# Kernel tuning notes

Measured on AMD Instinct MI355X. Metric: run time of the kernel, lower is better.

The kernel has to match this reference:

```python
import jax, jax.numpy as jnp
import numpy as np

C, DI, N, K, R = 64, 128, 16, 4, 4   # d_model, d_inner, d_state, d_conv, dt_rank
B, H, W = 4, 96, 96


def _layer_params(key):
    ks = jax.random.split(key, 6)
    p = {}
    p['ln_g'] = jnp.ones((C,), jnp.float32)
    p['ln_b'] = jnp.zeros((C,), jnp.float32)
    p['in_w'] = jax.random.normal(ks[0], (2 * DI, C), jnp.float32) / np.sqrt(C)
    p['conv_w'] = jax.random.normal(ks[1], (DI, K), jnp.float32) / np.sqrt(K)
    p['conv_b'] = jnp.zeros((DI,), jnp.float32)
    p['xp_w'] = jax.random.normal(ks[2], (R + 2 * N, DI), jnp.float32) / np.sqrt(DI)
    p['dt_w'] = jax.random.normal(ks[3], (DI, R), jnp.float32) / np.sqrt(R)
    p['dt_b'] = jnp.full((DI,), -4.0, jnp.float32)  # softplus(-4) ~ 0.018, sane dt
    p['A_log'] = jnp.broadcast_to(jnp.log(jnp.arange(1, N + 1, dtype=jnp.float32)), (DI, N)) + jnp.zeros((DI, N), jnp.float32)
    p['D'] = jnp.ones((DI,), jnp.float32)
    p['out_w'] = jax.random.normal(ks[4], (C, DI), jnp.float32) / np.sqrt(DI)
    p['skip'] = jnp.ones((1,), jnp.float32)
    p['pr_w'] = jax.random.normal(ks[5], (C, C), jnp.float32) / np.sqrt(C)
    p['pr_b'] = jnp.zeros((C,), jnp.float32)
    return p


def setup_inputs() -> dict:
    key = jax.random.key(0)
    k0, k1, k2 = jax.random.split(key, 3)
    inp = {'x': jax.random.normal(k0, (B, C, H, W), jnp.float32)}
    for i, k in ((1, k1), (2, k2)):
        for n, v in _layer_params(k).items():
            inp[f'{n}{i}'] = v
    return inp


def _silu(x):
    return x * jax.nn.sigmoid(x)


def _layer_norm(x, g, b, eps=1e-5):
    m = x.mean(-1, keepdims=True)
    v = x.var(-1, keepdims=True)
    return (x - m) * jax.lax.rsqrt(v + eps) * g + b


def _instance_norm(x, eps=1e-5):  # x: [B, C, H, W], no affine
    m = x.mean((2, 3), keepdims=True)
    v = x.var((2, 3), keepdims=True)
    return (x - m) * jax.lax.rsqrt(v + eps)


def _causal_conv(x, w, b):  # x: [B, L, D]; w: [D, K] depthwise; causal pad left
    L = x.shape[1]
    xp = jnp.pad(x, ((0, 0), (K - 1, 0), (0, 0)))
    y = b
    for k in range(K):
        y = y + xp[:, k:k + L, :] * w[:, k]
    return y


def _mamba(x, in_w, conv_w, conv_b, xp_w, dt_w, dt_b, A_log, Dp, out_w):
    # x: [B, L, C]
    xz = x @ in_w.T                       # [B, L, 2*DI]
    xin, z = jnp.split(xz, 2, axis=-1)
    xc = _silu(_causal_conv(xin, conv_w, conv_b))   # [B, L, DI]
    dbl = xc @ xp_w.T                     # [B, L, R + 2N]
    dt, Bm, Cm = jnp.split(dbl, [R, R + N], axis=-1)
    dt = jax.nn.softplus(dt @ dt_w.T + dt_b)        # [B, L, DI]
    A = -jnp.exp(A_log)                   # [DI, N]
    a = jnp.exp(dt[..., None] * A)                        # [B, L, DI, N]
    bb = dt[..., None] * Bm[:, :, None, :] * xc[..., None]  # [B, L, DI, N]

    def comb(l, r):
        a1, b1 = l
        a2, b2 = r
        return (a1 * a2, a2 * b1 + b2)

    _, h = jax.lax.associative_scan(comb, (a, bb), axis=1)  # h: [B, L, DI, N]
    y = jnp.einsum('bldn,bln->bld', h, Cm) + Dp * xc
    y = y * _silu(z)
    return y @ out_w.T                    # [B, L, C]


def _mamba_layer(x4, p):
    # x4: [B, C, H, W]
    b, c, h, w = x4.shape
    xf = x4.reshape(b, c, h * w).transpose(0, 2, 1)   # [B, L, C]
    xn = _layer_norm(xf, p['ln_g'], p['ln_b'])
    xm = _mamba(xn, p['in_w'], p['conv_w'], p['conv_b'], p['xp_w'], p['dt_w'],
                p['dt_b'], p['A_log'], p['D'], p['out_w']) + p['skip'] * xf
    xm = xm @ p['pr_w'].T + p['pr_b']
    return xm.transpose(0, 2, 1).reshape(b, c, h, w)


_PNAMES = ['ln_g', 'ln_b', 'in_w', 'conv_w', 'conv_b', 'xp_w', 'dt_w', 'dt_b',
           'A_log', 'D', 'out_w', 'skip', 'pr_w', 'pr_b']


def _forward(x, *ps):
    p1 = dict(zip(_PNAMES, ps[:14]))
    p2 = dict(zip(_PNAMES, ps[14:]))
    identity = x
    h = jax.nn.relu(_instance_norm(x))
    h = _mamba_layer(h, p1)
    h = jax.nn.relu(_instance_norm(h))
    h = _mamba_layer(h, p2)
    return h + identity


def reference(x, ln_g1, ln_b1, in_w1, conv_w1, conv_b1, xp_w1, dt_w1, dt_b1,
              A_log1, D1, out_w1, skip1, pr_w1, pr_b1,
              ln_g2, ln_b2, in_w2, conv_w2, conv_b2, xp_w2, dt_w2, dt_b2,
              A_log2, D2, out_w2, skip2, pr_w2, pr_b2):
    return _forward(x, ln_g1, ln_b1, in_w1, conv_w1, conv_b1, xp_w1, dt_w1, dt_b1,
                    A_log1, D1, out_w1, skip1, pr_w1, pr_b1,
                    ln_g2, ln_b2, in_w2, conv_w2, conv_b2, xp_w2, dt_w2, dt_b2,
                    A_log2, D2, out_w2, skip2, pr_w2, pr_b2)
```

## Files before the change

kernel.cpp:

```cpp
#include <hip/hip_runtime.h>
#include <math.h>

#define BB 4
#define CC 64
#define DI 128
#define NS 16
#define LL 9216
#define NT (LL / 64)

#define GCH 576
#define LCH 16
#define NSEQ 8192
#define SD  512
#define NG 24
#define GS 24

typedef __attribute__((ext_vector_type(8))) short bf16x8;
typedef __attribute__((ext_vector_type(4))) float fx4;
#define MFMA16 __builtin_amdgcn_mfma_f32_16x16x32_bf16

static __device__ __forceinline__ unsigned short f2b(float f) {
  unsigned u = __float_as_uint(f);
  u += 0x7fffu + ((u >> 16) & 1u);
  return (unsigned short)(u >> 16);
}
static __device__ __forceinline__ float b2f(unsigned short s) {
  return __uint_as_float(((unsigned)s) << 16);
}
static __device__ __forceinline__ float silu_f(float x) {
  return x / (1.f + __expf(-x));
}

static __device__ __forceinline__ void powers16(float e1, float* a) {
  float p2 = e1 * e1, p4 = p2 * p2, p8 = p4 * p4;
  a[0] = e1;      a[1] = p2;      a[2] = p2 * e1;      a[3] = p4;
  a[4] = p4 * e1; a[5] = p4 * p2; a[6] = p4 * p2 * e1; a[7] = p8;
  a[8] = p8 * e1; a[9] = p8 * p2; a[10] = p8 * p2 * e1; a[11] = p8 * p4;
  a[12] = p8 * p4 * e1; a[13] = p8 * p4 * p2; a[14] = p8 * p4 * p2 * e1; a[15] = p8 * p8;
}

static __device__ __forceinline__ float dt_and_a(float v, float A0, bool aone, bool afast,
                                                 const float* __restrict__ Alog, int d,
                                                 float* a) {
  float em = __expf(-fabsf(v));
  float t = 1.f + em;
  float dtv = fmaxf(v, 0.f) + __logf(t);
  if (aone) {
    float e1 = ((v >= 0.f) ? em : 1.f) / t;
    powers16(e1, a);
  } else if (afast) {
    powers16(__expf(dtv * A0), a);
  } else {
    #pragma unroll
    for (int n = 0; n < 16; ++n) a[n] = __expf(dtv * -__expf(Alog[d * NS + n]));
  }
  return dtv;
}

__global__ __launch_bounds__(256) void k_cvt(const float* __restrict__ inw1, const float* __restrict__ xpw1,
                                             const float* __restrict__ ow1, const float* __restrict__ pw1,
                                             const float* __restrict__ inw2, const float* __restrict__ xpw2,
                                             const float* __restrict__ ow2, const float* __restrict__ pw2,
                                             const float* __restrict__ alog1, const float* __restrict__ alog2,
                                             unsigned short* __restrict__ wb,
                                             float* __restrict__ prep) {
  int blk = blockIdx.x;
  int tid = threadIdx.x;
  if (blk >= 272) {
    int layer = blk - 272;
    const float* alog = layer ? alog2 : alog1;
    float* pr = prep + layer * 2304;
    #pragma unroll
    for (int j = 0; j < 8; ++j) {
      int e = tid + 256 * j;
      pr[e] = -__expf(alog[e]);
    }
    if (tid < 128) {
      int d = tid;
      float A0 = -__expf(alog[d * NS]);
      bool afast = true;
      #pragma unroll
      for (int n = 1; n < 16; ++n) {
        float An = -__expf(alog[d * NS + n]);
        afast = afast && (fabsf(An - A0 * (float)(n + 1)) <= 1e-3f * (float)(n + 1) * fabsf(A0));
      }
      bool aone = afast && (A0 == -1.0f);
      pr[2048 + d] = A0;
      pr[2176 + d] = aone ? 2.f : (afast ? 1.f : 0.f);
    }
    return;
  }
  int idx = blk * 256 + tid;
  int layer = idx >= 34816;
  int e = idx - layer * 34816;
  const float* inw = layer ? inw2 : inw1;
  const float* xpw = layer ? xpw2 : xpw1;
  const float* ow = layer ? ow2 : ow1;
  const float* pw = layer ? pw2 : pw1;
  float v;
  if (e < 16384) v = inw[e];
  else if (e < 22528) { int t = e - 16384; int r = t >> 7, c = t & 127; v = (r < 36) ? xpw[r * 128 + c] : 0.f; }
  else if (e < 30720) v = ow[e - 22528];
  else v = pw[e - 30720];
  wb[idx] = f2b(v);
}

__global__ __launch_bounds__(256) void k_stats(const float* __restrict__ p,
                                               float* __restrict__ stats) {
  int bc = blockIdx.x;
  const float* row = p + (size_t)bc * LL;
  float s = 0.f, s2 = 0.f;
  for (int i = threadIdx.x; i < LL; i += 256) {
    float v = row[i];
    s += v; s2 += v * v;
  }
  #pragma unroll
  for (int o = 32; o > 0; o >>= 1) {
    s += __shfl_down(s, o);
    s2 += __shfl_down(s2, o);
  }
  __shared__ float red[8];
  int w = threadIdx.x >> 6;
  if ((threadIdx.x & 63) == 0) { red[w] = s; red[4 + w] = s2; }
  __syncthreads();
  if (threadIdx.x == 0) {
    float S = red[0] + red[1] + red[2] + red[3];
    float S2 = red[4] + red[5] + red[6] + red[7];
    float m = S * (1.f / LL);
    float var = S2 * (1.f / LL) - m * m;
    stats[bc * 2] = m;
    stats[bc * 2 + 1] = rsqrtf(var + 1e-5f);
  }
}

__global__ __launch_bounds__(256) void k_fusein(const float* __restrict__ p,
                                                const float* __restrict__ stats,
                                                const float* __restrict__ g,
                                                const float* __restrict__ be,
                                                const unsigned short* __restrict__ w_b,
                                                unsigned short* __restrict__ xf_b,
                                                unsigned short* __restrict__ xin_b,
                                                unsigned short* __restrict__ sz_b) {
  int b = blockIdx.x / NT;
  int l0 = (blockIdx.x % NT) * 64;
  __shared__ float T[64][65];
  __shared__ unsigned short Tb[64][72];
  int li = threadIdx.x & 63;
  int c0 = threadIdx.x >> 6;
  #pragma unroll
  for (int j = 0; j < 16; ++j) {
    int c = c0 * 16 + j;
    float m = stats[(b * CC + c) * 2];
    float rs = stats[(b * CC + c) * 2 + 1];
    float v = p[((size_t)(b * CC + c)) * LL + l0 + li];
    T[li][c] = fmaxf((v - m) * rs, 0.f);
  }
  __syncthreads();
  {
    int row = threadIdx.x >> 2, part = threadIdx.x & 3;
    int ch0 = part * 16;
    float s = 0.f, s2 = 0.f;
    #pragma unroll
    for (int j = 0; j < 16; ++j) {
      float v = T[row][ch0 + j];
      s += v; s2 += v * v;
    }
    s += __shfl_xor(s, 1); s2 += __shfl_xor(s2, 1);
    s += __shfl_xor(s, 2); s2 += __shfl_xor(s2, 2);
    float m = s * (1.f / 64.f);
    float var = s2 * (1.f / 64.f) - m * m;
    float rs = rsqrtf(var + 1e-5f);
    size_t off0 = ((size_t)b * LL + l0 + row) * CC + ch0;
    #pragma unroll
    for (int j4 = 0; j4 < 4; ++j4) {
      float4 v4 = *(float4*)&T[row][ch0 + j4 * 4];
      xf_b[off0 + j4 * 4 + 0] = f2b(v4.x);
      xf_b[off0 + j4 * 4 + 1] = f2b(v4.y);
      xf_b[off0 + j4 * 4 + 2] = f2b(v4.z);
      xf_b[off0 + j4 * 4 + 3] = f2b(v4.w);
      float4 g4 = *(const float4*)&g[ch0 + j4 * 4];
      float4 b4 = *(const float4*)&be[ch0 + j4 * 4];
      Tb[row][ch0 + j4 * 4 + 0] = f2b((v4.x - m) * rs * g4.x + b4.x);
      Tb[row][ch0 + j4 * 4 + 1] = f2b((v4.y - m) * rs * g4.y + b4.y);
      Tb[row][ch0 + j4 * 4 + 2] = f2b((v4.z - m) * rs * g4.z + b4.z);
      Tb[row][ch0 + j4 * 4 + 3] = f2b((v4.w - m) * rs * g4.w + b4.w);
    }
  }
  __syncthreads();
  int lane = threadIdx.x & 63;
  int wv = threadIdx.x >> 6;
  int lr = lane & 15, kg = lane >> 4;
  int m0 = wv * 16;
  int rowg0 = blockIdx.x * 64 + m0;
  bf16x8 a0 = *(const bf16x8*)&Tb[m0 + lr][kg * 8];
  bf16x8 a1 = *(const bf16x8*)&Tb[m0 + lr][32 + kg * 8];
  #pragma unroll
  for (int nt = 0; nt < 16; ++nt) {
    bf16x8 b0 = *(const bf16x8*)&w_b[(size_t)(nt * 16 + lr) * CC + kg * 8];
    bf16x8 b1 = *(const bf16x8*)&w_b[(size_t)(nt * 16 + lr) * CC + 32 + kg * 8];
    fx4 c = {0.f, 0.f, 0.f, 0.f};
    c = MFMA16(a0, b0, c, 0, 0, 0);
    c = MFMA16(a1, b1, c, 0, 0, 0);
    #pragma unroll
    for (int r = 0; r < 4; ++r) {
      int row = rowg0 + kg * 4 + r, col = nt * 16 + lr;
      if (col < 128) xin_b[(size_t)row * DI + col] = f2b(c[r]);
      else           sz_b[(size_t)row * DI + col - 128] = f2b(silu_f(c[r]));
    }
  }
}

__global__ __launch_bounds__(128) void k_scanAX(const unsigned short* __restrict__ xin_b,
                                                const float* __restrict__ cw,
                                                const float* __restrict__ cb,
                                                const unsigned short* __restrict__ xpw_b,
                                                const float* __restrict__ Alog,
                                                const float* __restrict__ prep,
                                                const float* __restrict__ dtw,
                                                const float* __restrict__ dtbp,
                                                const float* __restrict__ Dp,
                                                float* __restrict__ dblC,
                                                float* __restrict__ dts,
                                                unsigned short* __restrict__ hlb,
                                                unsigned short* __restrict__ y1b,
                                                unsigned short* __restrict__ dtpreb) {
  int g = blockIdx.x % GCH;
  int b = blockIdx.x / GCH;
  __shared__ float dblP[2][16][40];
  __shared__ unsigned short xcS[16][136];
  int wv = threadIdx.x >> 6, lane = threadIdx.x & 63;
  int lr = lane & 15, kg = lane >> 4;
  {
    int lloc = g * LCH + lr;
    size_t row = (size_t)b * LL + lloc;
    const bf16x8 zv8 = {0, 0, 0, 0, 0, 0, 0, 0};
    fx4 acc[3];
    #pragma unroll
    for (int nt = 0; nt < 3; ++nt) acc[nt] = (fx4){0.f, 0.f, 0.f, 0.f};
    #pragma unroll
    for (int kk = 0; kk < 2; ++kk) {
      int cbase = (wv * 2 + kk) * 32 + kg * 8;
      bf16x8 x3 = *(const bf16x8*)&xin_b[row * DI + cbase];
      bf16x8 x2 = (lloc >= 1) ? *(const bf16x8*)&xin_b[(row - 1) * DI + cbase] : zv8;
      bf16x8 x1 = (lloc >= 2) ? *(const bf16x8*)&xin_b[(row - 2) * DI + cbase] : zv8;
      bf16x8 x0 = (lloc >= 3) ? *(const bf16x8*)&xin_b[(row - 3) * DI + cbase] : zv8;
      bf16x8 a;
      #pragma unroll
      for (int e = 0; e < 8; ++e) {
        int dd = cbase + e;
        float4 w4 = *(const float4*)&cw[dd * 4];
        float v = cb[dd] + b2f((unsigned short)x0[e]) * w4.x + b2f((unsigned short)x1[e]) * w4.y
                + b2f((unsigned short)x2[e]) * w4.z + b2f((unsigned short)x3[e]) * w4.w;
        a[e] = (short)f2b(silu_f(v));
      }
      *(bf16x8*)&xcS[lr][cbase] = a;
      #pragma unroll
      for (int nt = 0; nt < 3; ++nt) {
        bf16x8 bfr = *(const bf16x8*)&xpw_b[(size_t)(nt * 16 + lr) * DI + cbase];
        acc[nt] = MFMA16(a, bfr, acc[nt], 0, 0, 0);
      }
    }
    #pragma unroll
    for (int nt = 0; nt < 3; ++nt)
      #pragma unroll
      for (int r = 0; r < 4; ++r) {
        int col = nt * 16 + lr;
        if (col < 36) dblP[wv][kg * 4 + r][col] = acc[nt][r];
      }
  }
  __syncthreads();
  for (int e = threadIdx.x; e < 576; e += 128) {
    int r = e / 36, c = e - r * 36;
    dblP[0][r][c] += dblP[1][r][c];
  }
  __syncthreads();
  {
    size_t cbase16 = ((size_t)b * LL + g * LCH) * 16;
    #pragma unroll
    for (int j = 0; j < 2; ++j) {
      int e = threadIdx.x + 128 * j;
      dblC[cbase16 + e] = dblP[0][e >> 4][20 + (e & 15)];
    }
  }
  int d = threadIdx.x;
  float A0 = prep[2048 + d];
  int fl = (int)prep[2176 + d];
  bool afast = fl >= 1;
  bool aone = fl == 2;
  float4 w4 = *(const float4*)&dtw[d * 4];
  float dtbv = dtbp[d];
  float Dv = Dp[d];
  float h[16];
  #pragma unroll
  for (int n = 0; n < 16; ++n) h[n] = 0.f;
  float dtsum = 0.f;
  size_t sbase = ((size_t)b * LL + g * LCH) * DI + d;
  #pragma unroll 4
  for (int l = 0; l < LCH; ++l) {
    float xcv = b2f(xcS[l][d]);
    float4 qv = *(float4*)&dblP[0][l][0];
    float v = dtbv + qv.x * w4.x + qv.y * w4.y + qv.z * w4.z + qv.w * w4.w;
    float a[16];
    float dtv = dt_and_a(v, A0, aone, afast, Alog, d, a);
    float dx = dtv * xcv;
    dtsum += dtv;
    float4 b0 = *(float4*)&dblP[0][l][4];
    float4 b1 = *(float4*)&dblP[0][l][8];
    float4 b2 = *(float4*)&dblP[0][l][12];
    float4 b3 = *(float4*)&dblP[0][l][16];
    h[0]  = a[0]  * h[0]  + dx * b0.x;  h[1]  = a[1]  * h[1]  + dx * b0.y;
    h[2]  = a[2]  * h[2]  + dx * b0.z;  h[3]  = a[3]  * h[3]  + dx * b0.w;
    h[4]  = a[4]  * h[4]  + dx * b1.x;  h[5]  = a[5]  * h[5]  + dx * b1.y;
    h[6]  = a[6]  * h[6]  + dx * b1.z;  h[7]  = a[7]  * h[7]  + dx * b1.w;
    h[8]  = a[8]  * h[8]  + dx * b2.x;  h[9]  = a[9]  * h[9]  + dx * b2.y;
    h[10] = a[10] * h[10] + dx * b2.z;  h[11] = a[11] * h[11] + dx * b2.w;
    h[12] = a[12] * h[12] + dx * b3.x;  h[13] = a[13] * h[13] + dx * b3.y;
    h[14] = a[14] * h[14] + dx * b3.z;  h[15] = a[15] * h[15] + dx * b3.w;
    float4 cc0 = *(float4*)&dblP[0][l][20];
    float4 cc1 = *(float4*)&dblP[0][l][24];
    float4 cc2 = *(float4*)&dblP[0][l][28];
    float4 cc3 = *(float4*)&dblP[0][l][32];
    float y0 = h[0] * cc0.x + h[1] * cc0.y + h[2] * cc0.z + h[3] * cc0.w;
    float y1 = h[4] * cc1.x + h[5] * cc1.y + h[6] * cc1.z + h[7] * cc1.w;
    float y2 = h[8] * cc2.x + h[9] * cc2.y + h[10] * cc2.z + h[11] * cc2.w;
    float y3 = h[12] * cc3.x + h[13] * cc3.y + h[14] * cc3.z + h[15] * cc3.w;
    y1b[sbase + (size_t)l * DI] = f2b((y0 + y1) + (y2 + y3) + Dv * xcv);
    dtpreb[sbase + (size_t)l * DI] = f2b(dtsum);
  }
  dts[(size_t)g * SD + b * DI + d] = dtsum;
  size_t o = (size_t)g * NSEQ + ((size_t)b * DI + d) * NS;
  bf16x8 hv0, hv1;
  #pragma unroll
  for (int n = 0; n < 8; ++n) { hv0[n] = (short)f2b(h[n]); hv1[n] = (short)f2b(h[8 + n]); }
  *(bf16x8*)&hlb[o] = hv0;
  *(bf16x8*)&hlb[o + 8] = hv1;
}

__global__ __launch_bounds__(256) void k_scan2a(const float* __restrict__ dts,
                                                const unsigned short* __restrict__ hlb,
                                                const float* __restrict__ prep,
                                                float* __restrict__ gap,
                                                float* __restrict__ ghl) {
  int t = blockIdx.x * 256 + threadIdx.x;
  int grp = t >> 13, seq = t & (NSEQ - 1);
  int sd = seq >> 4;
  float An = prep[seq & (DI * NS - 1)];
  float A = 1.f, H = 0.f;
  int c0 = grp * GS;
  #pragma unroll 4
  for (int c = 0; c < GS; ++c) {
    float a = __expf(An * dts[(size_t)(c0 + c) * SD + sd]);
    H = a * H + b2f(hlb[(size_t)(c0 + c) * NSEQ + seq]);
    A *= a;
  }
  gap[t] = A;
  ghl[t] = H;
}

__global__ __launch_bounds__(256) void k_scan2bc(const float* __restrict__ dts,
                                                 const unsigned short* __restrict__ hlb,
                                                 const float* __restrict__ gap,
                                                 const float* __restrict__ ghl,
                                                 const float* __restrict__ prep,
                                                 unsigned short* __restrict__ hib) {
  int t = blockIdx.x * 256 + threadIdx.x;
  int grp = t >> 13, seq = t & (NSEQ - 1);
  int sd = seq >> 4;
  float An = prep[seq & (DI * NS - 1)];
  float h = 0.f;
  for (int gg = 0; gg < grp; ++gg)
    h = gap[gg * NSEQ + seq] * h + ghl[gg * NSEQ + seq];
  int c0 = grp * GS;
  #pragma unroll 4
  for (int c = 0; c < GS; ++c) {
    float a = __expf(An * dts[(size_t)(c0 + c) * SD + sd]);
    hib[(size_t)(c0 + c) * NSEQ + seq] = f2b(h);
    h = a * h + b2f(hlb[(size_t)(c0 + c) * NSEQ + seq]);
  }
}

__global__ __launch_bounds__(128) void k_scanCO(const float* __restrict__ dblC,
                                                const unsigned short* __restrict__ sz_b,
                                                const unsigned short* __restrict__ y1b,
                                                const unsigned short* __restrict__ dtpreb,
                                                const float* __restrict__ Alog,
                                                const float* __restrict__ prep,
                                                const unsigned short* __restrict__ hib,
                                                const unsigned short* __restrict__ ow_b,
                                                const unsigned short* __restrict__ xf_b,
                                                const float* __restrict__ skipv,
                                                const unsigned short* __restrict__ pw_b,
                                                const float* __restrict__ pb,
                                                const float* __restrict__ ident,
                                                float* __restrict__ dst, int addid) {
  int g = blockIdx.x % GCH;
  int b = blockIdx.x / GCH;
  int d = threadIdx.x;
  __shared__ float Cms[LCH * NS];
  __shared__ unsigned short yS[16][136];
  __shared__ unsigned short tmpS[16][72];
  {
    int tid = threadIdx.x;
    size_t cb16 = ((size_t)b * LL + g * LCH) * 16;
    if (tid < 64) *(float4*)&Cms[tid * 4] = *(const float4*)&dblC[cb16 + tid * 4];
  }
  float A0 = prep[2048 + d];
  bool afast = ((int)prep[2176 + d]) >= 1;
  __syncthreads();
  size_t o = (size_t)g * NSEQ + ((size_t)b * DI + d) * NS;
  float hiR[16];
  {
    bf16x8 h0 = *(const bf16x8*)&hib[o];
    bf16x8 h1 = *(const bf16x8*)&hib[o + 8];
    #pragma unroll
    for (int n = 0; n < 8; ++n) {
      hiR[n] = b2f((unsigned short)h0[n]);
      hiR[8 + n] = b2f((unsigned short)h1[n]);
    }
  }
  size_t base = ((size_t)b * LL + g * LCH) * DI + d;
  #pragma unroll 4
  for (int l = 0; l < LCH; ++l) {
    float dtpre = b2f(dtpreb[base + (size_t)l * DI]);
    float y1v = b2f(y1b[base + (size_t)l * DI]);
    float sg = b2f(sz_b[base + (size_t)l * DI]);
    float pw[16];
    if (afast) {
      powers16(__expf(A0 * dtpre), pw);
    } else {
      #pragma unroll
      for (int n = 0; n < 16; ++n) pw[n] = __expf(-__expf(Alog[d * NS + n]) * dtpre);
    }
    float4 c0 = *(float4*)&Cms[l * 16];
    float4 c1 = *(float4*)&Cms[l * 16 + 4];
    float4 c2 = *(float4*)&Cms[l * 16 + 8];
    float4 c3 = *(float4*)&Cms[l * 16 + 12];
    float s0 = c0.x * pw[0] * hiR[0] + c0.y * pw[1] * hiR[1] + c0.z * pw[2] * hiR[2] + c0.w * pw[3] * hiR[3];
    float s1 = c1.x * pw[4] * hiR[4] + c1.y * pw[5] * hiR[5] + c1.z * pw[6] * hiR[6] + c1.w * pw[7] * hiR[7];
    float s2 = c2.x * pw[8] * hiR[8] + c2.y * pw[9] * hiR[9] + c2.z * pw[10] * hiR[10] + c2.w * pw[11] * hiR[11];
    float s3 = c3.x * pw[12] * hiR[12] + c3.y * pw[13] * hiR[13] + c3.z * pw[14] * hiR[14] + c3.w * pw[15] * hiR[15];
    float yv = y1v + ((s0 + s1) + (s2 + s3));
    yS[l][d] = f2b(yv * sg);
  }
  __syncthreads();
  int lane = threadIdx.x & 63;
  int lr = lane & 15, kg = lane >> 4;
  int lw = threadIdx.x >> 6;
  {
    fx4 oacc[2];
    oacc[0] = (fx4){0.f, 0.f, 0.f, 0.f};
    oacc[1] = (fx4){0.f, 0.f, 0.f, 0.f};
    #pragma unroll
    for (int ks = 0; ks < 4; ++ks) {
      int cbase = ks * 32 + kg * 8;
      bf16x8 a = *(const bf16x8*)&yS[lr][cbase];
      #pragma unroll
      for (int j = 0; j < 2; ++j) {
        int nt = lw * 2 + j;
        bf16x8 bfr = *(const bf16x8*)&ow_b[(size_t)(nt * 16 + lr) * DI + cbase];
        oacc[j] = MFMA16(a, bfr, oacc[j], 0, 0, 0);
      }
    }
    float sk = skipv[0];
    #pragma unroll
    for (int j = 0; j < 2; ++j) {
      int nt = lw * 2 + j;
      #pragma unroll
      for (int r = 0; r < 4; ++r) {
        int rowl = kg * 4 + r, col = nt * 16 + lr;
        size_t grow = (size_t)b * LL + g * LCH + rowl;
        tmpS[rowl][col] = f2b(oacc[j][r] + sk * b2f(xf_b[grow * CC + col]));
      }
    }
  }
  __syncthreads();
  {
    fx4 pacc[2];
    pacc[0] = (fx4){0.f, 0.f, 0.f, 0.f};
    pacc[1] = (fx4){0.f, 0.f, 0.f, 0.f};
    #pragma unroll
    for (int ks = 0; ks < 2; ++ks) {
      int cbase = ks * 32 + kg * 8;
      bf16x8 bfrag = *(const bf16x8*)&tmpS[lr][cbase];
      #pragma unroll
      for (int j = 0; j < 2; ++j) {
        int ct = lw * 2 + j;
        bf16x8 a = *(const bf16x8*)&pw_b[(size_t)(ct * 16 + lr) * CC + cbase];
        pacc[j] = MFMA16(a, bfrag, pacc[j], 0, 0, 0);
      }
    }
    #pragma unroll
    for (int j = 0; j < 2; ++j) {
      int ct = lw * 2 + j;
      #pragma unroll
      for (int r = 0; r < 4; ++r) {
        int c = ct * 16 + kg * 4 + r;
        int lpos = g * LCH + lr;
        size_t off = ((size_t)(b * CC + c)) * LL + lpos;
        float val = pacc[j][r] + pb[c];
        if (addid) val += ident[off];
        dst[off] = val;
      }
    }
  }
}

extern "C" void kernel_launch(void* const* d_in, const int* in_sizes, int n_in,
                              void* d_out, int out_size, void* d_ws, size_t ws_size,
                              hipStream_t stream) {
  const float* x = (const float*)d_in[0];
  float* ws = (float*)d_ws;
  float* stats = ws;
  unsigned short* xf_b   = (unsigned short*)(ws + 1024);
  unsigned short* xin_b  = (unsigned short*)(ws + 1180672);
  unsigned short* sz_b   = (unsigned short*)(ws + 3539968);
  float* dblC  = ws + 5899264;
  float* dts   = ws + 6489088;
  unsigned short* hlb    = (unsigned short*)(ws + 6784000);
  unsigned short* hib    = (unsigned short*)(ws + 9143296);
  float* gap   = ws + 11502592;
  float* ghl   = ws + 11699200;
  unsigned short* wb     = (unsigned short*)(ws + 11895808);
  unsigned short* y1b    = (unsigned short*)(ws + 11930624);
  unsigned short* dtpreb = (unsigned short*)(ws + 14289920);
  float* prep  = ws + 16649216;
  float* inter = (float*)hlb;
  float* outp  = (float*)d_out;

  k_cvt<<<274, 256, 0, stream>>>((const float*)d_in[3], (const float*)d_in[6],
                                 (const float*)d_in[11], (const float*)d_in[13],
                                 (const float*)d_in[17], (const float*)d_in[20],
                                 (const float*)d_in[25], (const float*)d_in[27],
                                 (const float*)d_in[9], (const float*)d_in[23],
                                 wb, prep);

  const float* cur = x;
  for (int layer = 0; layer < 2; ++layer) {
    const int p0 = 1 + 14 * layer;
    const float* ln_g   = (const float*)d_in[p0 + 0];
    const float* ln_b   = (const float*)d_in[p0 + 1];
    const float* conv_w = (const float*)d_in[p0 + 3];
    const float* conv_b = (const float*)d_in[p0 + 4];
    const float* dt_w   = (const float*)d_in[p0 + 6];
    const float* dt_b   = (const float*)d_in[p0 + 7];
    const float* A_log  = (const float*)d_in[p0 + 8];
    const float* Dp     = (const float*)d_in[p0 + 9];
    const float* skip   = (const float*)d_in[p0 + 11];
    const float* pr_b   = (const float*)d_in[p0 + 13];
    const unsigned short* inw_b = wb + (size_t)layer * 34816;
    const unsigned short* xpw_b = inw_b + 16384;
    const unsigned short* ow_b  = inw_b + 22528;
    const unsigned short* pw_b  = inw_b + 30720;
    const float* prepL = prep + (size_t)layer * 2304;
    float* dst = (layer == 0) ? inter : outp;

    k_stats  <<<BB * CC, 256, 0, stream>>>(cur, stats);
    k_fusein <<<BB * NT, 256, 0, stream>>>(cur, stats, ln_g, ln_b, inw_b, xf_b, xin_b, sz_b);
    k_scanAX <<<BB * GCH, 128, 0, stream>>>(xin_b, conv_w, conv_b, xpw_b, A_log, prepL,
                                            dt_w, dt_b, Dp, dblC, dts, hlb, y1b, dtpreb);
    k_scan2a <<<(NG * NSEQ) / 256, 256, 0, stream>>>(dts, hlb, prepL, gap, ghl);
    k_scan2bc<<<(NG * NSEQ) / 256, 256, 0, stream>>>(dts, hlb, gap, ghl, prepL, hib);
    k_scanCO <<<BB * GCH, 128, 0, stream>>>(dblC, sz_b, y1b, dtpreb, A_log, prepL, hib,
                                            ow_b, xf_b, skip, pw_b, pr_b, x, dst, layer);
    cur = inter;
  }
}
```

Measured before the change: 208.2 us.

## Fuse instance-norm statistics into weight-convert and scan output kernels

The first layer's per-channel mean and rstd are now computed by extra blocks in the weight-conversion kernel, so the separate stats pass over the input runs alongside it. For the second layer, the output kernel of layer one writes per-chunk partial sums and sums of squares, and a small finalize kernel reduces them. This removes a full re-read of the intermediate activation and one launch per layer. The cost is extra shuffles and partial-sum writes in the scan output epilogue, a new workspace buffer, and a different summation order in the statistics.

```diff
diff --git a/kernel.cpp b/kernel.cpp
--- a/kernel.cpp
+++ b/kernel.cpp
@@ -62,10 +62,39 @@
                                              const float* __restrict__ inw2, const float* __restrict__ xpw2,
                                              const float* __restrict__ ow2, const float* __restrict__ pw2,
                                              const float* __restrict__ alog1, const float* __restrict__ alog2,
+                                             const float* __restrict__ x,
                                              unsigned short* __restrict__ wb,
-                                             float* __restrict__ prep) {
+                                             float* __restrict__ prep,
+                                             float* __restrict__ stats) {
   int blk = blockIdx.x;
   int tid = threadIdx.x;
+  if (blk >= 274) {
+    int bc = blk - 274;
+    const float* row = x + (size_t)bc * LL;
+    float s = 0.f, s2 = 0.f;
+    for (int i = tid; i < LL; i += 256) {
+      float v = row[i];
+      s += v; s2 += v * v;
+    }
+    #pragma unroll
+    for (int o = 32; o > 0; o >>= 1) {
+      s += __shfl_down(s, o);
+      s2 += __shfl_down(s2, o);
+    }
+    __shared__ float red[8];
+    int w = tid >> 6;
+    if ((tid & 63) == 0) { red[w] = s; red[4 + w] = s2; }
+    __syncthreads();
+    if (tid == 0) {
+      float S = red[0] + red[1] + red[2] + red[3];
+      float S2 = red[4] + red[5] + red[6] + red[7];
+      float m = S * (1.f / LL);
+      float var = S2 * (1.f / LL) - m * m;
+      stats[bc * 2] = m;
+      stats[bc * 2 + 1] = rsqrtf(var + 1e-5f);
+    }
+    return;
+  }
   if (blk >= 272) {
     int layer = blk - 272;
     const float* alog = layer ? alog2 : alog1;
@@ -105,27 +134,23 @@
   wb[idx] = f2b(v);
 }
 
-__global__ __launch_bounds__(256) void k_stats(const float* __restrict__ p,
-                                               float* __restrict__ stats) {
+__global__ __launch_bounds__(64) void k_statfin(const float* __restrict__ partials,
+                                                float* __restrict__ stats) {
   int bc = blockIdx.x;
-  const float* row = p + (size_t)bc * LL;
-  float s = 0.f, s2 = 0.f;
-  for (int i = threadIdx.x; i < LL; i += 256) {
-    float v = row[i];
-    s += v; s2 += v * v;
+  int b = bc >> 6, c = bc & 63;
+  int t = threadIdx.x;
+  float S = 0.f, S2 = 0.f;
+  for (int g = t; g < GCH; g += 64) {
+    size_t pbase = ((size_t)(b * GCH + g)) * 128 + c * 2;
+    S += partials[pbase];
+    S2 += partials[pbase + 1];
   }
   #pragma unroll
   for (int o = 32; o > 0; o >>= 1) {
-    s += __shfl_down(s, o);
-    s2 += __shfl_down(s2, o);
-  }
-  __shared__ float red[8];
-  int w = threadIdx.x >> 6;
-  if ((threadIdx.x & 63) == 0) { red[w] = s; red[4 + w] = s2; }
-  __syncthreads();
-  if (threadIdx.x == 0) {
-    float S = red[0] + red[1] + red[2] + red[3];
-    float S2 = red[4] + red[5] + red[6] + red[7];
+    S += __shfl_down(S, o);
+    S2 += __shfl_down(S2, o);
+  }
+  if (t == 0) {
     float m = S * (1.f / LL);
     float var = S2 * (1.f / LL) - m * m;
     stats[bc * 2] = m;
@@ -392,6 +417,7 @@
                                                 const unsigned short* __restrict__ pw_b,
                                                 const float* __restrict__ pb,
                                                 const float* __restrict__ ident,
+                                                float* __restrict__ partials,
                                                 float* __restrict__ dst, int addid) {
   int g = blockIdx.x % GCH;
   int b = blockIdx.x / GCH;
@@ -498,8 +524,21 @@
         int lpos = g * LCH + lr;
         size_t off = ((size_t)(b * CC + c)) * LL + lpos;
         float val = pacc[j][r] + pb[c];
-        if (addid) val += ident[off];
-        dst[off] = val;
+        if (addid) {
+          dst[off] = val + ident[off];
+        } else {
+          dst[off] = val;
+          float s = val, s2 = val * val;
+          s += __shfl_xor(s, 1); s2 += __shfl_xor(s2, 1);
+          s += __shfl_xor(s, 2); s2 += __shfl_xor(s2, 2);
+          s += __shfl_xor(s, 4); s2 += __shfl_xor(s2, 4);
+          s += __shfl_xor(s, 8); s2 += __shfl_xor(s2, 8);
+          if (lr == 0) {
+            size_t pbase = ((size_t)(b * GCH + g)) * 128 + c * 2;
+            partials[pbase] = s;
+            partials[pbase + 1] = s2;
+          }
+        }
       }
     }
   }
@@ -524,15 +563,16 @@
   unsigned short* y1b    = (unsigned short*)(ws + 11930624);
   unsigned short* dtpreb = (unsigned short*)(ws + 14289920);
   float* prep  = ws + 16649216;
+  float* partials = ws + 16653824;
   float* inter = (float*)hlb;
   float* outp  = (float*)d_out;
 
-  k_cvt<<<274, 256, 0, stream>>>((const float*)d_in[3], (const float*)d_in[6],
+  k_cvt<<<530, 256, 0, stream>>>((const float*)d_in[3], (const float*)d_in[6],
                                  (const float*)d_in[11], (const float*)d_in[13],
                                  (const float*)d_in[17], (const float*)d_in[20],
                                  (const float*)d_in[25], (const float*)d_in[27],
                                  (const float*)d_in[9], (const float*)d_in[23],
-                                 wb, prep);
+                                 x, wb, prep, stats);
 
   const float* cur = x;
   for (int layer = 0; layer < 2; ++layer) {
@@ -554,14 +594,16 @@
     const float* prepL = prep + (size_t)layer * 2304;
     float* dst = (layer == 0) ? inter : outp;
 
-    k_stats  <<<BB * CC, 256, 0, stream>>>(cur, stats);
     k_fusein <<<BB * NT, 256, 0, stream>>>(cur, stats, ln_g, ln_b, inw_b, xf_b, xin_b, sz_b);
     k_scanAX <<<BB * GCH, 128, 0, stream>>>(xin_b, conv_w, conv_b, xpw_b, A_log, prepL,
                                             dt_w, dt_b, Dp, dblC, dts, hlb, y1b, dtpreb);
     k_scan2a <<<(NG * NSEQ) / 256, 256, 0, stream>>>(dts, hlb, prepL, gap, ghl);
     k_scan2bc<<<(NG * NSEQ) / 256, 256, 0, stream>>>(dts, hlb, gap, ghl, prepL, hib);
     k_scanCO <<<BB * GCH, 128, 0, stream>>>(dblC, sz_b, y1b, dtpreb, A_log, prepL, hib,
-                                            ow_b, xf_b, skip, pw_b, pr_b, x, dst, layer);
+                                            ow_b, xf_b, skip, pw_b, pr_b, x, partials,
+                                            dst, layer);
+    if (layer == 0)
+      k_statfin<<<BB * CC, 64, 0, stream>>>(partials, stats);
     cur = inter;
   }
 }
```

Measured after the change: 200.5 us. 1.04x faster.
